# Kernel tuning notes

Measured on AMD Instinct MI355X. Metric: run time of the kernel, lower is better.

The kernel has to match this reference:

```python
import jax, jax.numpy as jnp
import numpy as np

B, S, D = 16, 2048, 128

def setup_inputs() -> dict:
    key = jax.random.key(0)
    kq, kk, kv, km = jax.random.split(key, 4)
    Q = jax.random.normal(kq, (B, S, D), dtype=jnp.float32)
    K = jax.random.normal(kk, (B, S, D), dtype=jnp.float32)
    V = jax.random.normal(kv, (B, S, D), dtype=jnp.float32)
    # mask: True entries are masked out (filled with -inf), same as torch.masked_fill_
    mask = jax.random.randint(km, (B, S, S), 0, 2).astype(bool)
    return {"Q": Q, "K": K, "V": V, "mask": mask, "dk": 128}

def reference(Q, K, V, mask, dk):
    # scores: [B, S_q, S_k]
    w = jnp.einsum('bqd,bkd->bqk', Q, K)
    w = jnp.where(mask, -jnp.inf, w)
    # scale applied to masked scores (as in original: mask first, then divide);
    # -inf / scale stays -inf, so math matches exactly.
    scale = jnp.asarray(dk, w.dtype) ** 0.5
    p = jax.nn.softmax(w / scale, axis=-1)
    # context: [B, S_q, D]
    return jnp.einsum('bqk,bkd->bqd', p, V)
```

## Files before the change

### kernel.cpp

```cpp
#include <hip/hip_runtime.h>
#include <hip/hip_bf16.h>
#include <stdint.h>

typedef __attribute__((ext_vector_type(8)))  short short8;
typedef __attribute__((ext_vector_type(4)))  float floatx4;
typedef __attribute__((ext_vector_type(16))) float floatx16;

#define S_LEN 2048
#define DH    128
#define BQ    64
#define BKV   64
#define NSTEP (S_LEN / BKV)
#define SCALE 0.08838834764831845f
#define SCALE2 0.12753785429791905f
#define DTHR 11.541560327111708f

__device__ __forceinline__ float ex2(float x) { return __builtin_amdgcn_exp2f(x); }

__device__ __forceinline__ unsigned short f2b(float f) {
    union { float f; unsigned u; } v; v.f = f;
    unsigned r = v.u + 0x7fffu + ((v.u >> 16) & 1u);
    return (unsigned short)(r >> 16);
}

__device__ __forceinline__ unsigned cvt_pk(float lo, float hi) {
    unsigned r;
    asm("v_cvt_pk_bf16_f32 %0, %1, %2" : "=v"(r) : "v"(lo), "v"(hi));
    return r;
}


__global__ __launch_bounds__(256) void kfrag_make(const float* __restrict__ K,
                                                  unsigned short* __restrict__ KF)
{
    const int T = blockIdx.x, b = blockIdx.y;
    const float* Kb = K + ((size_t)b * S_LEN + T * 64) * DH;
    unsigned short* out = KF + ((size_t)(b * 32 + T)) * 1024 * 8;
    #pragma unroll
    for (int i = 0; i < 4; ++i) {
        int F = i * 256 + threadIdx.x;
        int lq = F & 31, h = (F >> 5) & 1, dsub = (F >> 6) & 7, wk = F >> 9;
        const float* src = Kb + (size_t)(wk * 32 + lq) * DH + dsub * 16 + h * 8;
        float4 a = *(const float4*)src, bb = *(const float4*)(src + 4);
        short8 f;
        f[0] = f2b(a.x);  f[1] = f2b(a.y);  f[2] = f2b(a.z);  f[3] = f2b(a.w);
        f[4] = f2b(bb.x); f[5] = f2b(bb.y); f[6] = f2b(bb.z); f[7] = f2b(bb.w);
        *(short8*)(out + (size_t)F * 8) = f;
    }
}

__global__ __launch_bounds__(256) void vfrag_make(const float* __restrict__ V,
                                                  unsigned short* __restrict__ VF)
{
    __shared__ float t[32][33];
    const int k0 = blockIdx.x * 32, d0 = blockIdx.y * 32, b = blockIdx.z;
    const int tx = threadIdx.x & 31, ty = threadIdx.x >> 5;
    const float* Vb = V + ((size_t)b * S_LEN + k0) * DH + d0;
    #pragma unroll
    for (int i = 0; i < 4; ++i)
        t[ty + 8 * i][tx] = Vb[(size_t)(ty + 8 * i) * DH + tx];
    __syncthreads();
    if (threadIdx.x < 128) {
        const int lq = threadIdx.x & 31;
        const int h  = (threadIdx.x >> 5) & 1;
        const int ks = threadIdx.x >> 6;
        const int T = k0 >> 6, wk = (k0 >> 5) & 1, ds = d0 >> 5;
        short8 f;
        #pragma unroll
        for (int e = 0; e < 8; ++e)
            f[e] = f2b(t[ks * 16 + h * 8 + e][lq]);
        unsigned short* o = VF +
            ((((((size_t)(b * 32 + T) * 4 + ds) * 2 + wk) * 2 + ks) * 2 + h) * 32 + lq) * 8;
        *(short8*)o = f;
    }
}

__global__ __launch_bounds__(256) void pack_mask(const int* __restrict__ M,
                                                 unsigned long long* __restrict__ P)
{
    const int lane = threadIdx.x & 63;
    const int wv   = threadIdx.x >> 6;
    const int row  = blockIdx.x * 4 + wv;
    const int* Mr  = M + (size_t)row * S_LEN;
    unsigned long long* Pr = P + (size_t)row * 32;
    #pragma unroll
    for (int it = 0; it < 8; ++it) {
        int4 v = *(const int4*)(Mr + it * 256 + lane * 4);
        unsigned long long b0 = __ballot(v.x != 0);
        unsigned long long b1 = __ballot(v.y != 0);
        unsigned long long b2 = __ballot(v.z != 0);
        unsigned long long b3 = __ballot(v.w != 0);
        if (lane == 0) {
            Pr[it * 4 + 0] = b0;
            Pr[it * 4 + 1] = b1;
            Pr[it * 4 + 2] = b2;
            Pr[it * 4 + 3] = b3;
        }
    }
}

#define LDS_BYTES 34816

__global__ __launch_bounds__(256, 2)
void attn_fwd(const float* __restrict__ Q, const unsigned short* __restrict__ KF,
              const unsigned short* __restrict__ VF,
              const unsigned long long* __restrict__ Pm,
              float* __restrict__ O)
{
    __shared__ __align__(128) char lds[LDS_BYTES];

    const int tid  = threadIdx.x;
    const int lane = tid & 63;
    const int w    = tid >> 6;
    const int wq   = w & 1;
    const int wk   = w >> 1;
    const int lq   = lane & 31;
    const int hi   = lane >> 5;
    const int qt   = blockIdx.x;
    const int b    = blockIdx.y;
    const int q0   = qt * BQ;

    short8 qf[8];
    {
        const float* qrow = Q + ((size_t)(b * S_LEN + q0 + wq * 32 + lq)) * DH;
        #pragma unroll
        for (int dsub = 0; dsub < 8; ++dsub) {
            const float* p = qrow + dsub * 16 + hi * 8;
            float4 a  = *(const float4*)(p);
            float4 bb = *(const float4*)(p + 4);
            short8 f;
            f[0] = f2b(a.x * SCALE2);  f[1] = f2b(a.y * SCALE2);
            f[2] = f2b(a.z * SCALE2);  f[3] = f2b(a.w * SCALE2);
            f[4] = f2b(bb.x * SCALE2); f[5] = f2b(bb.y * SCALE2);
            f[6] = f2b(bb.z * SCALE2); f[7] = f2b(bb.w * SCALE2);
            qf[dsub] = f;
        }
    }

    float m_run = -1e30f;
    float l_run = 0.f;
    floatx16 accO[4];
    #pragma unroll
    for (int i = 0; i < 4; ++i) accO[i] = (floatx16)(0.f);

    const unsigned short* KFl = KF + (((size_t)(b * 32) * 2 + wk) * 512
                                      + (size_t)hi * 32 + lq) * 8;
    const unsigned short* VFl = VF + ((((size_t)(b * 32) * 4 * 2 + wk) * 2) * 2 * 32
                                      + (size_t)hi * 32 + lq) * 8;

    const unsigned long long* Pk = Pm
        + ((size_t)(b * S_LEN + q0 + wq * 32 + lq) << 5);

    unsigned long long mgc[4], mgn[4];
    short8 kfA[8], kfB[8], vfc[8];

#define LOAD_MG(DST, G) {                                                     \
    ulonglong2 a_ = *(const ulonglong2*)(Pk + (G) * 4);                       \
    ulonglong2 b_ = *(const ulonglong2*)(Pk + (G) * 4 + 2);                   \
    DST[0] = a_.x; DST[1] = a_.y; DST[2] = b_.x; DST[3] = b_.y; }

#define LOAD_KF(DST, T) {                                                     \
    const unsigned short* kp_ = KFl + (size_t)(T) * (2 * 512 * 8);            \
    _Pragma("unroll")                                                         \
    for (int dsub = 0; dsub < 8; ++dsub)                                      \
        DST[dsub] = *(const short8*)(kp_ + dsub * 512);                       \
}

#define LOAD_VF(T) {                                                          \
    _Pragma("unroll")                                                         \
    for (int ds = 0; ds < 4; ++ds)                                            \
        _Pragma("unroll")                                                     \
        for (int ks = 0; ks < 2; ++ks)                                        \
            vfc[ds * 2 + ks] = *(const short8*)(VFl                           \
                + ((size_t)(T) * 16 + ds * 4 + ks) * (2 * 32 * 8));           \
}

    LOAD_KF(kfA, 0);
    LOAD_MG(mgc, 0);
    LOAD_MG(mgn, 1);

#define STEP_BODY(T, TT, KFC, KFN) {                                          \
    if ((T) + 1 < NSTEP) LOAD_KF(KFN, (T) + 1);                               \
    LOAD_VF(T);                                                               \
                                                                    \
    floatx16 accS = (floatx16)(0.f);                                          \
    __builtin_amdgcn_s_setprio(1);                                            \
    _Pragma("unroll")                                                         \
    for (int dsub = 0; dsub < 8; ++dsub)                                      \
        accS = __builtin_amdgcn_mfma_f32_32x32x16_bf16(                       \
                   KFC[dsub], qf[dsub], accS, 0, 0, 0);                       \
    __builtin_amdgcn_s_setprio(0);                                            \
                                           \
    const int base_ = (TT) * 16 + wk * 8 + hi;                                \
    unsigned mb0 = (unsigned)(mgc[0] >> base_);                               \
    unsigned mb1 = (unsigned)(mgc[1] >> base_);                               \
    unsigned mb2 = (unsigned)(mgc[2] >> base_);                               \
    unsigned mb3 = (unsigned)(mgc[3] >> base_);                               \
    float p_[16];                                                             \
    _Pragma("unroll")                                                         \
    for (int j = 0; j < 4; ++j) {                                             \
        p_[4*j+0] = ((mb0 >> (2*j)) & 1u) ? -1e30f : accS[4*j+0];             \
        p_[4*j+1] = ((mb1 >> (2*j)) & 1u) ? -1e30f : accS[4*j+1];             \
        p_[4*j+2] = ((mb2 >> (2*j)) & 1u) ? -1e30f : accS[4*j+2];             \
        p_[4*j+3] = ((mb3 >> (2*j)) & 1u) ? -1e30f : accS[4*j+3];             \
    }                                                                         \
    float mx = p_[0];                                                         \
    _Pragma("unroll")                                                         \
    for (int r = 1; r < 16; ++r) mx = fmaxf(mx, p_[r]);                       \
    mx = fmaxf(mx, __shfl_xor(mx, 32));                                       \
    int need = __any(mx - m_run > DTHR);                                      \
    float corr = 1.0f;                                                        \
    if (need) {                                                               \
        float mn = fmaxf(m_run, mx);                                          \
        corr = ex2(m_run - mn);                                               \
        m_run = mn;                                                           \
    }                                                                         \
    float ts = 0.f;                                                           \
    _Pragma("unroll")                                                         \
    for (int r = 0; r < 16; ++r) { p_[r] = ex2(p_[r] - m_run); ts += p_[r]; } \
    ts += __shfl_xor(ts, 32);                                                 \
    if (need) {                                                               \
        l_run = l_run * corr + ts;                                            \
        _Pragma("unroll")                                                     \
        for (int ds = 0; ds < 4; ++ds) {                                      \
            floatx16 o = accO[ds];                                            \
            _Pragma("unroll")                                                 \
            for (int r = 0; r < 16; ++r) o[r] *= corr;                        \
            accO[ds] = o;                                                     \
        }                                                                     \
    } else {                                                                  \
        l_run += ts;                                                          \
    }                                                                         \
                                 \
    short8 pf[2];                                                             \
    _Pragma("unroll")                                                         \
    for (int ks = 0; ks < 2; ++ks) {                                          \
        unsigned a01 = cvt_pk(p_[8*ks+0], p_[8*ks+1]);                        \
        unsigned a23 = cvt_pk(p_[8*ks+2], p_[8*ks+3]);                        \
        unsigned b01 = cvt_pk(p_[8*ks+4], p_[8*ks+5]);                        \
        unsigned b23 = cvt_pk(p_[8*ks+6], p_[8*ks+7]);                        \
        unsigned ta01 = (unsigned)__shfl_xor((int)a01, 32);                   \
        unsigned ta23 = (unsigned)__shfl_xor((int)a23, 32);                   \
        unsigned tb01 = (unsigned)__shfl_xor((int)b01, 32);                   \
        unsigned tb23 = (unsigned)__shfl_xor((int)b23, 32);                   \
        union { unsigned u[4]; short8 v; } pu;                                \
        pu.u[0] = hi ? tb01 : a01;                                            \
        pu.u[1] = hi ? tb23 : a23;                                            \
        pu.u[2] = hi ? b01 : ta01;                                            \
        pu.u[3] = hi ? b23 : ta23;                                            \
        pf[ks] = pu.v;                                                        \
    }                                                                         \
                                                                      \
    __builtin_amdgcn_s_setprio(1);                                            \
    _Pragma("unroll")                                                         \
    for (int ds = 0; ds < 4; ++ds)                                            \
        _Pragma("unroll")                                                     \
        for (int ks = 0; ks < 2; ++ks)                                        \
            accO[ds] = __builtin_amdgcn_mfma_f32_32x32x16_bf16(               \
                           vfc[ds * 2 + ks], pf[ks], accO[ds], 0, 0, 0);      \
    __builtin_amdgcn_s_setprio(0);                                            \
}

    for (int g = 0; g < 8; ++g) {
        STEP_BODY(4 * g + 0, 0, kfA, kfB)
        STEP_BODY(4 * g + 1, 1, kfB, kfA)
        STEP_BODY(4 * g + 2, 2, kfA, kfB)
        STEP_BODY(4 * g + 3, 3, kfB, kfA)
        mgc[0] = mgn[0]; mgc[1] = mgn[1]; mgc[2] = mgn[2]; mgc[3] = mgn[3];
        if (g + 2 < 8) LOAD_MG(mgn, g + 2);
    }
#undef STEP_BODY
#undef LOAD_KF
#undef LOAD_VF
#undef LOAD_MG

    {
        float* mg = (float*)lds;
        const int slot = (wq * 64 + lane) * 68;
        if (wk == 1) {
            #pragma unroll
            for (int ds = 0; ds < 4; ++ds)
                #pragma unroll
                for (int rr = 0; rr < 4; ++rr) {
                    float4 v;
                    v.x = accO[ds][4*rr+0]; v.y = accO[ds][4*rr+1];
                    v.z = accO[ds][4*rr+2]; v.w = accO[ds][4*rr+3];
                    *(float4*)(mg + slot + ds * 16 + rr * 4) = v;
                }
            mg[slot + 64] = m_run;
            mg[slot + 65] = l_run;
        }
        __syncthreads();
        if (wk == 0) {
            float m1 = mg[slot + 64], l1 = mg[slot + 65];
            float m  = fmaxf(m_run, m1);
            float f0 = ex2(m_run - m), f1 = ex2(m1 - m);
            float l  = l_run * f0 + l1 * f1;
            float inv = (l > 0.f) ? 1.f / l : 0.f;
            float* Ob = O + ((size_t)(b * S_LEN + q0 + wq * 32 + lq)) * DH;
            #pragma unroll
            for (int ds = 0; ds < 4; ++ds)
                #pragma unroll
                for (int rr = 0; rr < 4; ++rr) {
                    float4 part = *(const float4*)(mg + slot + ds * 16 + rr * 4);
                    float4 ov;
                    ov.x = (accO[ds][4*rr+0] * f0 + part.x * f1) * inv;
                    ov.y = (accO[ds][4*rr+1] * f0 + part.y * f1) * inv;
                    ov.z = (accO[ds][4*rr+2] * f0 + part.z * f1) * inv;
                    ov.w = (accO[ds][4*rr+3] * f0 + part.w * f1) * inv;
                    *(float4*)(Ob + ds * 32 + 8 * rr + 4 * hi) = ov;
                }
        }
    }
}

#define FB_LDS_BYTES 77824

__global__ __launch_bounds__(256, 2)
void attn_fwd_fb(const float* __restrict__ Q, const float* __restrict__ K,
                 const float* __restrict__ V, const int* __restrict__ M,
                 float* __restrict__ O)
{
    __shared__ __align__(128) char lds[FB_LDS_BYTES];

    const int tid  = threadIdx.x;
    const int lane = tid & 63;
    const int w    = tid >> 6;
    const int c    = lane & 15;
    const int g    = lane >> 4;
    const int qt   = blockIdx.x;
    const int b    = blockIdx.y;
    const int q0   = qt * 64;

    const int rbase = tid >> 5;
    const int c4    = tid & 31;
    const unsigned swk = (unsigned)(c4 * 8) ^ (unsigned)(rbase << 4);
    const int vd    = tid & 127;
    const int vk0   = (tid >> 7) * 32;

    short8 qf[4];
    {
        const float* qrow = Q + ((size_t)(b * S_LEN + q0 + w * 16 + c)) * DH;
        #pragma unroll
        for (int dk = 0; dk < 4; ++dk) {
            const float* p = qrow + dk * 32 + g * 8;
            float4 a  = *(const float4*)(p);
            float4 bb = *(const float4*)(p + 4);
            short8 f;
            f[0] = f2b(a.x * SCALE);  f[1] = f2b(a.y * SCALE);
            f[2] = f2b(a.z * SCALE);  f[3] = f2b(a.w * SCALE);
            f[4] = f2b(bb.x * SCALE); f[5] = f2b(bb.y * SCALE);
            f[6] = f2b(bb.z * SCALE); f[7] = f2b(bb.w * SCALE);
            qf[dk] = f;
        }
    }

    float m_run[4] = {-1e30f, -1e30f, -1e30f, -1e30f};
    float l_run[4] = {0.f, 0.f, 0.f, 0.f};
    floatx4 accO[8];
    #pragma unroll
    for (int i = 0; i < 8; ++i) accO[i] = (floatx4)(0.f);

    const float* Kb = K + (size_t)b * S_LEN * DH;
    const float* Vb = V + (size_t)b * S_LEN * DH;
    const int*   Mb = M + (size_t)b * S_LEN * S_LEN + (size_t)q0 * S_LEN;

    size_t moff[4];
    #pragma unroll
    for (int r = 0; r < 4; ++r)
        moff[r] = (size_t)(w * 16 + 4 * g + r) * S_LEN;

    float4 kreg[8];
    float  vreg[32];
    int    mreg[16];

    #pragma unroll
    for (int i = 0; i < 8; ++i)
        kreg[i] = *(const float4*)(Kb + (size_t)(i * 8 + rbase) * DH + c4 * 4);
    #pragma unroll
    for (int j = 0; j < 32; ++j)
        vreg[j] = Vb[(size_t)(vk0 + j) * DH + vd];
    #pragma unroll
    for (int r = 0; r < 4; ++r)
        #pragma unroll
        for (int n = 0; n < 4; ++n)
            mreg[r * 4 + n] = Mb[moff[r] + n * 16 + c];

    #pragma unroll
    for (int i = 0; i < 8; ++i) {
        float4 kv = kreg[i];
        unsigned long long kp =
              (unsigned long long)f2b(kv.x)
            | ((unsigned long long)f2b(kv.y) << 16)
            | ((unsigned long long)f2b(kv.z) << 32)
            | ((unsigned long long)f2b(kv.w) << 48);
        *(unsigned long long*)(lds + (i * 8 + rbase) * 256 + swk) = kp;
    }
    {
        char* vbase = lds + 32768 + vd * 144 + vk0 * 2;
        #pragma unroll
        for (int i = 0; i < 4; ++i) {
            short8 pk;
            #pragma unroll
            for (int e = 0; e < 8; ++e) pk[e] = f2b(vreg[i * 8 + e]);
            *(short8*)(vbase + i * 16) = pk;
        }
    }
    #pragma unroll
    for (int i = 0; i < 8; ++i)
        kreg[i] = *(const float4*)(Kb + (size_t)(BKV + i * 8 + rbase) * DH + c4 * 4);
    #pragma unroll
    for (int j = 0; j < 32; ++j)
        vreg[j] = Vb[(size_t)(BKV + vk0 + j) * DH + vd];

    __syncthreads();

    char* psw = lds + 69632 + w * 2048;

    for (int step = 0; step < NSTEP; ++step) {
        const int p = step & 1;
        const int kv0 = step * BKV;
        char* KHp = lds + p * 16384;
        char* VTp = lds + 32768 + p * 18432;

        floatx4 accS[4];
        #pragma unroll
        for (int n = 0; n < 4; ++n) accS[n] = (floatx4)(0.f);
        #pragma unroll
        for (int n = 0; n < 4; ++n) {
            const char* krow = KHp + (n * 16 + c) * 256;
            #pragma unroll
            for (int dk = 0; dk < 4; ++dk) {
                unsigned colb = (unsigned)(dk * 64 + g * 16) ^ (unsigned)((c & 7) << 4);
                short8 kf = *(const short8*)(krow + colb);
                accS[n] = __builtin_amdgcn_mfma_f32_16x16x32_bf16(qf[dk], kf, accS[n], 0, 0, 0);
            }
        }

        float pv[4][4];
        float corr[4];
        #pragma unroll
        for (int r = 0; r < 4; ++r) {
            float sv[4];
            #pragma unroll
            for (int n = 0; n < 4; ++n) {
                float s = accS[n][r];
                if (mreg[r * 4 + n]) s = -1e30f;
                sv[n] = s;
            }
            float tm = fmaxf(fmaxf(sv[0], sv[1]), fmaxf(sv[2], sv[3]));
            #pragma unroll
            for (int off = 1; off < 16; off <<= 1)
                tm = fmaxf(tm, __shfl_xor(tm, off, 64));
            float mn = fmaxf(m_run[r], tm);
            corr[r]  = __expf(m_run[r] - mn);
            m_run[r] = mn;
            float ts = 0.f;
            #pragma unroll
            for (int n = 0; n < 4; ++n) { pv[n][r] = __expf(sv[n] - mn); ts += pv[n][r]; }
            #pragma unroll
            for (int off = 1; off < 16; off <<= 1)
                ts += __shfl_xor(ts, off, 64);
            l_run[r] = l_run[r] * corr[r] + ts;
        }
        if (step + 1 < NSTEP) {
            const int kvn = kv0 + BKV;
            #pragma unroll
            for (int r = 0; r < 4; ++r)
                #pragma unroll
                for (int n = 0; n < 4; ++n)
                    mreg[r * 4 + n] = Mb[moff[r] + kvn + n * 16 + c];
        }

        #pragma unroll
        for (int s8 = 0; s8 < 8; ++s8) {
            floatx4 o = accO[s8];
            o[0] *= corr[0]; o[1] *= corr[1]; o[2] *= corr[2]; o[3] *= corr[3];
            accO[s8] = o;
        }

        #pragma unroll
        for (int r = 0; r < 4; ++r) {
            int rl = 4 * g + r;
            #pragma unroll
            for (int n = 0; n < 4; ++n) {
                unsigned colb = (unsigned)((n * 16 + c) * 2) ^ (unsigned)((rl & 7) << 4);
                *(unsigned short*)(psw + rl * 128 + colb) = f2b(pv[n][r]);
            }
        }

        #pragma unroll
        for (int sub = 0; sub < 2; ++sub) {
            unsigned colb = (unsigned)(sub * 64 + g * 16) ^ (unsigned)((c & 7) << 4);
            short8 pf = *(const short8*)(psw + c * 128 + colb);
            #pragma unroll
            for (int s8 = 0; s8 < 8; ++s8) {
                short8 vf = *(const short8*)(VTp + (s8 * 16 + c) * 144 + sub * 64 + g * 16);
                accO[s8] = __builtin_amdgcn_mfma_f32_16x16x32_bf16(pf, vf, accO[s8], 0, 0, 0);
            }
        }

        if (step + 1 < NSTEP) {
            char* KHn = lds + (p ^ 1) * 16384;
            char* VTn = lds + 32768 + (p ^ 1) * 18432;
            #pragma unroll
            for (int i = 0; i < 8; ++i) {
                float4 kv = kreg[i];
                unsigned long long kp =
                      (unsigned long long)f2b(kv.x)
                    | ((unsigned long long)f2b(kv.y) << 16)
                    | ((unsigned long long)f2b(kv.z) << 32)
                    | ((unsigned long long)f2b(kv.w) << 48);
                *(unsigned long long*)(KHn + (i * 8 + rbase) * 256 + swk) = kp;
            }
            char* vbase = VTn + vd * 144 + vk0 * 2;
            #pragma unroll
            for (int i = 0; i < 4; ++i) {
                short8 pk;
                #pragma unroll
                for (int e = 0; e < 8; ++e) pk[e] = f2b(vreg[i * 8 + e]);
                *(short8*)(vbase + i * 16) = pk;
            }
            if (step + 2 < NSTEP) {
                const int kvn2 = kv0 + 2 * BKV;
                #pragma unroll
                for (int i = 0; i < 8; ++i)
                    kreg[i] = *(const float4*)(Kb + (size_t)(kvn2 + i * 8 + rbase) * DH + c4 * 4);
                #pragma unroll
                for (int j = 0; j < 32; ++j)
                    vreg[j] = Vb[(size_t)(kvn2 + vk0 + j) * DH + vd];
            }
        }
        __syncthreads();
    }

    float inv[4];
    #pragma unroll
    for (int r = 0; r < 4; ++r) inv[r] = (l_run[r] > 0.f) ? 1.f / l_run[r] : 0.f;
    float* Ob = O + ((size_t)(b * S_LEN + q0 + w * 16)) * DH;
    #pragma unroll
    for (int s8 = 0; s8 < 8; ++s8) {
        #pragma unroll
        for (int r = 0; r < 4; ++r) {
            Ob[(size_t)(4 * g + r) * DH + s8 * 16 + c] = accO[s8][r] * inv[r];
        }
    }
}

extern "C" void kernel_launch(void* const* d_in, const int* in_sizes, int n_in,
                              void* d_out, int out_size, void* d_ws, size_t ws_size,
                              hipStream_t stream) {
    const float* Q = (const float*)d_in[0];
    const float* K = (const float*)d_in[1];
    const float* V = (const float*)d_in[2];
    const int*   M = (const int*)d_in[3];
    float*       O = (float*)d_out;

    const size_t elems    = (size_t)16 * S_LEN * DH;
    const size_t kv_bytes = elems * sizeof(unsigned short);
    const size_t pm_bytes = (size_t)16 * S_LEN * 32 * 8;
    if (ws_size >= 2 * kv_bytes + pm_bytes) {
        unsigned short*     KF = (unsigned short*)d_ws;
        unsigned short*     VF = (unsigned short*)d_ws + elems;
        unsigned long long* Pm = (unsigned long long*)((char*)d_ws + 2 * kv_bytes);
        kfrag_make<<<dim3(32, 16), dim3(256), 0, stream>>>(K, KF);
        vfrag_make<<<dim3(S_LEN / 32, DH / 32, 16), dim3(256), 0, stream>>>(V, VF);
        pack_mask<<<dim3(16 * S_LEN / 4), dim3(256), 0, stream>>>(M, Pm);
        attn_fwd<<<dim3(S_LEN / BQ, 16), dim3(256), 0, stream>>>(Q, KF, VF, Pm, O);
    } else {
        attn_fwd_fb<<<dim3(S_LEN / 64, 16), dim3(256), 0, stream>>>(Q, K, V, M, O);
    }
}
```

Measured before the change: 123.5 us.

## Drop mask pre-packing kernel and read int mask directly in attention

Removes the separate pack_mask kernel that turned the int mask into bitmasks. The attention kernel now loads int4 mask words straight from the original mask, prefetching two KV steps ahead in double-buffered registers. This saves a kernel launch and the write-then-read of the packed mask. In exchange each query block reads the full 32-bit mask (about 32x more mask traffic in the main kernel, no longer amortized) and uses more registers, which may lower occupancy.

```diff
diff --git a/kernel.cpp b/kernel.cpp
--- a/kernel.cpp
+++ b/kernel.cpp
@@ -75,36 +75,12 @@
     }
 }
 
-__global__ __launch_bounds__(256) void pack_mask(const int* __restrict__ M,
-                                                 unsigned long long* __restrict__ P)
-{
-    const int lane = threadIdx.x & 63;
-    const int wv   = threadIdx.x >> 6;
-    const int row  = blockIdx.x * 4 + wv;
-    const int* Mr  = M + (size_t)row * S_LEN;
-    unsigned long long* Pr = P + (size_t)row * 32;
-    #pragma unroll
-    for (int it = 0; it < 8; ++it) {
-        int4 v = *(const int4*)(Mr + it * 256 + lane * 4);
-        unsigned long long b0 = __ballot(v.x != 0);
-        unsigned long long b1 = __ballot(v.y != 0);
-        unsigned long long b2 = __ballot(v.z != 0);
-        unsigned long long b3 = __ballot(v.w != 0);
-        if (lane == 0) {
-            Pr[it * 4 + 0] = b0;
-            Pr[it * 4 + 1] = b1;
-            Pr[it * 4 + 2] = b2;
-            Pr[it * 4 + 3] = b3;
-        }
-    }
-}
-
 #define LDS_BYTES 34816
 
 __global__ __launch_bounds__(256, 2)
 void attn_fwd(const float* __restrict__ Q, const unsigned short* __restrict__ KF,
               const unsigned short* __restrict__ VF,
-              const unsigned long long* __restrict__ Pm,
+              const int* __restrict__ M,
               float* __restrict__ O)
 {
     __shared__ __align__(128) char lds[LDS_BYTES];
@@ -148,16 +124,18 @@
     const unsigned short* VFl = VF + ((((size_t)(b * 32) * 4 * 2 + wk) * 2) * 2 * 32
                                       + (size_t)hi * 32 + lq) * 8;
 
-    const unsigned long long* Pk = Pm
-        + ((size_t)(b * S_LEN + q0 + wq * 32 + lq) << 5);
-
-    unsigned long long mgc[4], mgn[4];
+    const int* Mrow = M + (size_t)b * S_LEN * S_LEN
+                        + (size_t)(q0 + wq * 32 + lq) * S_LEN + wk * 32 + 4 * hi;
+
+    int4 mA[4], mB[4];
     short8 kfA[8], kfB[8], vfc[8];
 
-#define LOAD_MG(DST, G) {                                                     \
-    ulonglong2 a_ = *(const ulonglong2*)(Pk + (G) * 4);                       \
-    ulonglong2 b_ = *(const ulonglong2*)(Pk + (G) * 4 + 2);                   \
-    DST[0] = a_.x; DST[1] = a_.y; DST[2] = b_.x; DST[3] = b_.y; }
+#define LOAD_MASK(DST, T) {                                                   \
+    const int* mp_ = Mrow + (T) * 64;                                         \
+    DST[0] = *(const int4*)(mp_);                                             \
+    DST[1] = *(const int4*)(mp_ + 8);                                         \
+    DST[2] = *(const int4*)(mp_ + 16);                                        \
+    DST[3] = *(const int4*)(mp_ + 24); }
 
 #define LOAD_KF(DST, T) {                                                     \
     const unsigned short* kp_ = KFl + (size_t)(T) * (2 * 512 * 8);            \
@@ -176,10 +154,10 @@
 }
 
     LOAD_KF(kfA, 0);
-    LOAD_MG(mgc, 0);
-    LOAD_MG(mgn, 1);
-
-#define STEP_BODY(T, TT, KFC, KFN) {                                          \
+    LOAD_MASK(mA, 0);
+    LOAD_MASK(mB, 1);
+
+#define STEP_BODY(T, KFC, KFN, MCUR) {                                        \
     if ((T) + 1 < NSTEP) LOAD_KF(KFN, (T) + 1);                               \
     LOAD_VF(T);                                                               \
                                                                     \
@@ -190,20 +168,18 @@
         accS = __builtin_amdgcn_mfma_f32_32x32x16_bf16(                       \
                    KFC[dsub], qf[dsub], accS, 0, 0, 0);                       \
     __builtin_amdgcn_s_setprio(0);                                            \
-                                           \
-    const int base_ = (TT) * 16 + wk * 8 + hi;                                \
-    unsigned mb0 = (unsigned)(mgc[0] >> base_);                               \
-    unsigned mb1 = (unsigned)(mgc[1] >> base_);                               \
-    unsigned mb2 = (unsigned)(mgc[2] >> base_);                               \
-    unsigned mb3 = (unsigned)(mgc[3] >> base_);                               \
+                  \
     float p_[16];                                                             \
     _Pragma("unroll")                                                         \
     for (int j = 0; j < 4; ++j) {                                             \
-        p_[4*j+0] = ((mb0 >> (2*j)) & 1u) ? -1e30f : accS[4*j+0];             \
-        p_[4*j+1] = ((mb1 >> (2*j)) & 1u) ? -1e30f : accS[4*j+1];             \
-        p_[4*j+2] = ((mb2 >> (2*j)) & 1u) ? -1e30f : accS[4*j+2];             \
-        p_[4*j+3] = ((mb3 >> (2*j)) & 1u) ? -1e30f : accS[4*j+3];             \
+        int4 mm = MCUR[j];                                                    \
+        p_[4*j+0] = mm.x ? -1e30f : accS[4*j+0];                              \
+        p_[4*j+1] = mm.y ? -1e30f : accS[4*j+1];                              \
+        p_[4*j+2] = mm.z ? -1e30f : accS[4*j+2];                              \
+        p_[4*j+3] = mm.w ? -1e30f : accS[4*j+3];                              \
     }                                                                         \
+     \
+    if ((T) + 2 < NSTEP) LOAD_MASK(MCUR, (T) + 2);                            \
     float mx = p_[0];                                                         \
     _Pragma("unroll")                                                         \
     for (int r = 1; r < 16; ++r) mx = fmaxf(mx, p_[r]);                       \
@@ -261,18 +237,14 @@
     __builtin_amdgcn_s_setprio(0);                                            \
 }
 
-    for (int g = 0; g < 8; ++g) {
-        STEP_BODY(4 * g + 0, 0, kfA, kfB)
-        STEP_BODY(4 * g + 1, 1, kfB, kfA)
-        STEP_BODY(4 * g + 2, 2, kfA, kfB)
-        STEP_BODY(4 * g + 3, 3, kfB, kfA)
-        mgc[0] = mgn[0]; mgc[1] = mgn[1]; mgc[2] = mgn[2]; mgc[3] = mgn[3];
-        if (g + 2 < 8) LOAD_MG(mgn, g + 2);
+    for (int t = 0; t < NSTEP; t += 2) {
+        STEP_BODY(t,     kfA, kfB, mA)
+        STEP_BODY(t + 1, kfB, kfA, mB)
     }
 #undef STEP_BODY
 #undef LOAD_KF
 #undef LOAD_VF
-#undef LOAD_MG
+#undef LOAD_MASK
 
     {
         float* mg = (float*)lds;
@@ -558,15 +530,12 @@
 
     const size_t elems    = (size_t)16 * S_LEN * DH;
     const size_t kv_bytes = elems * sizeof(unsigned short);
-    const size_t pm_bytes = (size_t)16 * S_LEN * 32 * 8;
-    if (ws_size >= 2 * kv_bytes + pm_bytes) {
-        unsigned short*     KF = (unsigned short*)d_ws;
-        unsigned short*     VF = (unsigned short*)d_ws + elems;
-        unsigned long long* Pm = (unsigned long long*)((char*)d_ws + 2 * kv_bytes);
-        kfrag_make<<<dim3(32, 16), dim3(256), 0, stream>>>(K, KF);
-        vfrag_make<<<dim3(S_LEN / 32, DH / 32, 16), dim3(256), 0, stream>>>(V, VF);
-        pack_mask<<<dim3(16 * S_LEN / 4), dim3(256), 0, stream>>>(M, Pm);
-        attn_fwd<<<dim3(S_LEN / BQ, 16), dim3(256), 0, stream>>>(Q, KF, VF, Pm, O);
+    if (ws_size >= 2 * kv_bytes) {
+        unsigned short* KFp = (unsigned short*)d_ws;
+        unsigned short* VFp = (unsigned short*)d_ws + elems;
+        kfrag_make<<<dim3(32, 16), dim3(256), 0, stream>>>(K, KFp);
+        vfrag_make<<<dim3(S_LEN / 32, DH / 32, 16), dim3(256), 0, stream>>>(V, VFp);
+        attn_fwd<<<dim3(S_LEN / BQ, 16), dim3(256), 0, stream>>>(Q, KFp, VFp, M, O);
     } else {
         attn_fwd_fb<<<dim3(S_LEN / 64, 16), dim3(256), 0, stream>>>(Q, K, V, M, O);
     }
```

After: 160.9 us. 1.3x slower.
